# Kernel tuning notes

Measured on AMD Instinct MI355X. Metric: run time of the kernel, lower is better.

The kernel has to match this reference:

```python
import jax, jax.numpy as jnp
import numpy as np

N_NODES = 100000
N_EDGES = 1600000
IN_DIM = 16
HID = 128
N_LAYERS = 3
LN_EPS = 1e-5


def setup_inputs() -> dict:
    key = jax.random.key(0)
    ks = jax.random.split(key, 8)
    x = jax.random.normal(ks[0], (N_NODES, IN_DIM), dtype=jnp.float32)
    edge_index = jax.random.randint(ks[1], (2, N_EDGES), 0, N_NODES, dtype=jnp.int64)
    # input projection params
    W_in = jax.random.normal(ks[2], (IN_DIM, HID), dtype=jnp.float32) * (1.0 / np.sqrt(IN_DIM))
    b_in = jnp.zeros((HID,), dtype=jnp.float32)
    # stacked GCNConv weights [L, H, H] and biases [L, H]
    W_conv = jax.random.normal(ks[3], (N_LAYERS, HID, HID), dtype=jnp.float32) * (1.0 / np.sqrt(HID))
    b_conv = jnp.zeros((N_LAYERS, HID), dtype=jnp.float32)
    # LayerNorm params [L, H]
    ln_gamma = jnp.ones((N_LAYERS, HID), dtype=jnp.float32)
    ln_beta = jnp.zeros((N_LAYERS, HID), dtype=jnp.float32)
    return {"x": x, "edge_index": edge_index, "W_in": W_in, "b_in": b_in,
            "W_conv": W_conv, "b_conv": b_conv, "ln_gamma": ln_gamma, "ln_beta": ln_beta}


def _layer_norm(h, gamma, beta):
    mu = jnp.mean(h, axis=-1, keepdims=True)
    var = jnp.mean(jnp.square(h - mu), axis=-1, keepdims=True)
    return (h - mu) * jax.lax.rsqrt(var + LN_EPS) * gamma + beta


def reference(x, edge_index, W_in, b_in, W_conv, b_conv, ln_gamma, ln_beta):
    N = x.shape[0]
    loops = jnp.arange(N, dtype=edge_index.dtype)
    src = jnp.concatenate([edge_index[0], loops])  # add self-loops (GCNConv default)
    dst = jnp.concatenate([edge_index[1], loops])
    # symmetric normalization D^-1/2 (A+I) D^-1/2
    deg = jax.ops.segment_sum(jnp.ones(src.shape[0], dtype=x.dtype), dst, num_segments=N)
    dis = jax.lax.rsqrt(jnp.maximum(deg, 1.0))  # deg >= 1 with self-loops
    coef = (dis[src] * dis[dst])[:, None]  # [E+N, 1]
    h = x @ W_in + b_in  # input projection -> [N, HID]
    for l in range(N_LAYERS):
        h_prev = h
        m = h @ W_conv[l]  # transform then propagate (same math as GCNConv)
        agg = jax.ops.segment_sum(m[src] * coef, dst, num_segments=N) + b_conv[l]
        h = jax.nn.relu(_layer_norm(agg, ln_gamma[l], ln_beta[l]))
        if l > 0:  # residual only for i > 0, dims always match
            h = h + h_prev
    return h
```

## Files before the change

### kernel.cpp

```cpp
#include <hip/hip_runtime.h>
#include <hip/hip_bf16.h>
#include <hip/hip_fp16.h>

#define HID 128
#define BCHUNK 4096

typedef __attribute__((ext_vector_type(8))) short short8;
typedef __attribute__((ext_vector_type(4))) float f32x4;

__device__ __forceinline__ float ldf(const void* p, size_t i, int bf16f) {
    if (bf16f) {
        unsigned short u = ((const unsigned short*)p)[i];
        union { unsigned int x; float f; } v; v.x = ((unsigned int)u) << 16;
        return v.f;
    }
    return ((const float*)p)[i];
}
__device__ __forceinline__ int ld_idx(const void* p, size_t i, int i64f) {
    return i64f ? (int)((const long long*)p)[i] : ((const int*)p)[i];
}
__device__ __forceinline__ unsigned short f2bfu(float f) {
    __hip_bfloat16 h = __float2bfloat16(f);
    return *reinterpret_cast<unsigned short*>(&h);
}
__device__ __forceinline__ float bfbits(unsigned int lo16) {
    union { unsigned int x; float f; } v; v.x = lo16 << 16;
    return v.f;
}

__global__ void k_detect(const void* __restrict__ gamma, const void* __restrict__ ei,
                         int* flags) {
    if (threadIdx.x == 0 && blockIdx.x == 0) {
        unsigned int g0 = ((const unsigned int*)gamma)[0];
        flags[0] = (g0 != 0x3F800000u) ? 1 : 0;
        const unsigned int* e32 = (const unsigned int*)ei;
        int i64 = 1;
        for (int k = 0; k < 128; k++)
            if (e32[2 * k + 1] != 0u) { i64 = 0; break; }
        flags[1] = i64;
    }
}

__global__ void k_zero(int* p, int n) {
    int i = blockIdx.x * blockDim.x + threadIdx.x;
    if (i < n) p[i] = 0;
}

__global__ __launch_bounds__(256) void k_bucket(const void* __restrict__ ei,
                                                int E, int N, int nbk, int cap,
                                                int* bkcur, unsigned* __restrict__ bdata,
                                                const int* __restrict__ flags) {
    __shared__ int hist[512], base[512];
    int i64 = flags[1];
    int t = threadIdx.x;
    for (int i = t; i < nbk; i += 256) hist[i] = 0;
    __syncthreads();
    int e0 = blockIdx.x * BCHUNK;
    int ss[16], dd[16];
#pragma unroll
    for (int k = 0; k < 16; k++) {
        int e = e0 + k * 256 + t;
        dd[k] = -1;
        if (e < E) {
            int d = ld_idx(ei, (size_t)E + e, i64);
            int s = ld_idx(ei, e, i64);
            if ((unsigned)d < (unsigned)N && (unsigned)s < (unsigned)N) {
                dd[k] = d; ss[k] = s;
                atomicAdd(&hist[d >> 9], 1);
            }
        }
    }
    __syncthreads();
    for (int i = t; i < nbk; i += 256) {
        int c = hist[i];
        base[i] = c ? atomicAdd(&bkcur[i], c) : 0;
        hist[i] = 0;
    }
    __syncthreads();
#pragma unroll
    for (int k = 0; k < 16; k++) {
        if (dd[k] >= 0) {
            int b = dd[k] >> 9;
            int pos = base[b] + atomicAdd(&hist[b], 1);
            if (pos < cap)
                bdata[(size_t)b * cap + pos] =
                    (unsigned)ss[k] | ((unsigned)(dd[k] & 511) << 17);
        }
    }
}

__global__ void k_bkscan(const int* __restrict__ bkcur, int* bkpre, int nbk,
                         int* row_ptr, int N, int cap) {
    if (threadIdx.x == 0 && blockIdx.x == 0) {
        int run = 0;
        for (int b = 0; b < nbk; b++) {
            bkpre[b] = run;
            run += min(bkcur[b], cap);
        }
        row_ptr[N] = run;
    }
}

__global__ __launch_bounds__(256) void k_bhist(const int* __restrict__ bkcur,
                                               const int* __restrict__ bkpre,
                                               const unsigned* __restrict__ bdata,
                                               int cap, int* __restrict__ row_ptr,
                                               float* __restrict__ dis, int N) {
    __shared__ int hist[512];
    __shared__ int lsum;
    int b = blockIdx.x, t = threadIdx.x;
    for (int i = t; i < 512; i += 256) hist[i] = 0;
    __syncthreads();
    int cb = min(bkcur[b], cap);
    for (int k = t; k < cb; k += 256)
        atomicAdd(&hist[bdata[(size_t)b * cap + k] >> 17], 1);
    __syncthreads();
    int v0 = hist[t], v1 = hist[256 + t];
    int s0 = v0, s1 = v1;
    for (int off = 1; off < 256; off <<= 1) {
        int x0 = (t >= off) ? hist[t - off] : 0;
        int x1 = (t >= off) ? hist[256 + t - off] : 0;
        __syncthreads();
        s0 += x0; s1 += x1;
        hist[t] = s0; hist[256 + t] = s1;
        __syncthreads();
    }
    if (t == 255) lsum = s0;
    __syncthreads();
    int nbase = b << 9;
    int base = bkpre[b];
    if (nbase + t < N) {
        row_ptr[nbase + t] = base + s0 - v0;
        dis[nbase + t] = rsqrtf((float)(v0 + 1));
    }
    if (nbase + 256 + t < N) {
        row_ptr[nbase + 256 + t] = base + lsum + s1 - v1;
        dis[nbase + 256 + t] = rsqrtf((float)(v1 + 1));
    }
}

__global__ __launch_bounds__(256) void k_bfill(const int* __restrict__ bkcur,
                                               const unsigned* __restrict__ bdata,
                                               int cap, const int* __restrict__ row_ptr,
                                               int* __restrict__ csr_src, int N) {
    __shared__ int cur[512];
    int b = blockIdx.x, t = threadIdx.x;
    for (int i = t; i < 512; i += 256) cur[i] = 0;
    __syncthreads();
    int cb = min(bkcur[b], cap);
    int nbase = b << 9;
    for (int k = t; k < cb; k += 256) {
        unsigned u = bdata[(size_t)b * cap + k];
        int dl = u >> 17;
        int j = row_ptr[nbase + dl] + atomicAdd(&cur[dl], 1);
        csr_src[j] = (int)(u & 0x1FFFFu);
    }
}

__global__ void k_wtrans(const void* __restrict__ W, unsigned short* __restrict__ Wt,
                         const int* __restrict__ flags) {
    int bf = flags[0];
    int l = blockIdx.x >> 7, n = blockIdx.x & 127, k = threadIdx.x;
    float w = ldf(W, (size_t)l * 16384 + (size_t)k * 128 + n, bf);
    Wt[(size_t)l * 16384 + (size_t)n * 128 + k] = f2bfu(w);
}

__global__ void k_proj(const void* __restrict__ x, const void* __restrict__ Win,
                       const void* __restrict__ bin,
                       unsigned short* __restrict__ hb, int N,
                       const int* __restrict__ flags) {
    int bf = flags[0];
    int node = blockIdx.x;
    int t = threadIdx.x;
    __shared__ float xs[16];
    if (t < 16) xs[t] = ldf(x, (size_t)node * 16 + t, bf);
    __syncthreads();
    float acc = ldf(bin, t, bf);
#pragma unroll
    for (int k = 0; k < 16; k++)
        acc += xs[k] * ldf(Win, (size_t)k * HID + t, bf);
    hb[(size_t)node * HID + t] = f2bfu(acc);
}

__global__ __launch_bounds__(256) void k_gemm(const unsigned short* __restrict__ hb,
                                              const unsigned short* __restrict__ Wt,
                                              unsigned short* __restrict__ m, int N,
                                              int ntiles) {
    int t = threadIdx.x;
    int wave = t >> 6, lane = t & 63;
    int quad = lane >> 4, n15 = lane & 15;
    short8 bfr[4][8];
#pragma unroll
    for (int kc = 0; kc < 4; kc++)
#pragma unroll
        for (int nt = 0; nt < 8; nt++)
            bfr[kc][nt] = *(const short8*)(Wt + (size_t)(nt * 16 + n15) * HID +
                                           kc * 32 + quad * 8);
    int wid = blockIdx.x * 4 + wave;
    int nwaves = gridDim.x * 4;
    for (int tile = wid; tile < ntiles; tile += nwaves) {
        int row0 = tile * 16;
        int arow = min(row0 + n15, N - 1);
        const short8* ap = (const short8*)(hb + (size_t)arow * HID + quad * 8);
        short8 a0 = ap[0], a1 = ap[4], a2 = ap[8], a3 = ap[12];
        f32x4 acc[8] = {};
#pragma unroll
        for (int nt = 0; nt < 8; nt++) {
            acc[nt] = __builtin_amdgcn_mfma_f32_16x16x32_bf16(a0, bfr[0][nt], acc[nt], 0, 0, 0);
            acc[nt] = __builtin_amdgcn_mfma_f32_16x16x32_bf16(a1, bfr[1][nt], acc[nt], 0, 0, 0);
            acc[nt] = __builtin_amdgcn_mfma_f32_16x16x32_bf16(a2, bfr[2][nt], acc[nt], 0, 0, 0);
            acc[nt] = __builtin_amdgcn_mfma_f32_16x16x32_bf16(a3, bfr[3][nt], acc[nt], 0, 0, 0);
        }
#pragma unroll
        for (int nt = 0; nt < 8; nt++)
#pragma unroll
            for (int r = 0; r < 4; r++) {
                int row = row0 + quad * 4 + r;
                if (row < N)
                    m[(size_t)row * HID + nt * 16 + n15] = f2bfu(acc[nt][r]);
            }
    }
}

__global__ __launch_bounds__(256) void k_layer(
        const int* __restrict__ row_ptr, const int* __restrict__ csr_src,
        const unsigned int* __restrict__ m2, const float* __restrict__ dis,
        const void* __restrict__ bc, size_t boff,
        const void* __restrict__ lg, const void* __restrict__ lb, size_t goff,
        unsigned int* __restrict__ hb, void* __restrict__ out, int N,
        int res, int last, const int* __restrict__ flags) {
    int t = threadIdx.x, wave = t >> 6, lane = t & 63;
    int node = blockIdx.x * 4 + wave;
    if (node >= N) return;
    int bf = flags[0];
    float dn = dis[node], dd = dn * dn;
    unsigned int ms = m2[(size_t)node * 64 + lane];
    float v0 = ldf(bc, boff + 2 * lane, bf)     + bfbits(ms & 0xffffu) * dd;
    float v1 = ldf(bc, boff + 2 * lane + 1, bf) + bfbits(ms >> 16) * dd;
    int beg = row_ptr[node], end = row_ptr[node + 1];
    float p0 = 0.f, p1 = 0.f, q0 = 0.f, q1 = 0.f, r0 = 0.f, r1 = 0.f;
    int j = beg;
    for (; j + 3 < end; j += 4) {
        int s0 = csr_src[j], s1 = csr_src[j + 1];
        int s2 = csr_src[j + 2], s3 = csr_src[j + 3];
        float c0 = dis[s0] * dn, c1 = dis[s1] * dn;
        float c2 = dis[s2] * dn, c3 = dis[s3] * dn;
        unsigned int u0 = m2[(size_t)s0 * 64 + lane];
        unsigned int u1 = m2[(size_t)s1 * 64 + lane];
        unsigned int u2 = m2[(size_t)s2 * 64 + lane];
        unsigned int u3 = m2[(size_t)s3 * 64 + lane];
        v0 += bfbits(u0 & 0xffffu) * c0; v1 += bfbits(u0 >> 16) * c0;
        p0 += bfbits(u1 & 0xffffu) * c1; p1 += bfbits(u1 >> 16) * c1;
        q0 += bfbits(u2 & 0xffffu) * c2; q1 += bfbits(u2 >> 16) * c2;
        r0 += bfbits(u3 & 0xffffu) * c3; r1 += bfbits(u3 >> 16) * c3;
    }
    for (; j < end; j++) {
        int s0 = csr_src[j];
        float c0 = dis[s0] * dn;
        unsigned int u0 = m2[(size_t)s0 * 64 + lane];
        v0 += bfbits(u0 & 0xffffu) * c0; v1 += bfbits(u0 >> 16) * c0;
    }
    v0 += p0 + q0 + r0;
    v1 += p1 + q1 + r1;
    float s1 = v0 + v1, s2 = v0 * v0 + v1 * v1;
#pragma unroll
    for (int o = 32; o; o >>= 1) {
        s1 += __shfl_down(s1, o);
        s2 += __shfl_down(s2, o);
    }
    float sum = __shfl(s1, 0), sq = __shfl(s2, 0);
    float mu = sum * (1.0f / HID);
    float var = sq * (1.0f / HID) - mu * mu;
    float r = rsqrtf(var + 1e-5f);
    float g0 = ldf(lg, goff + 2 * lane, bf), g1 = ldf(lg, goff + 2 * lane + 1, bf);
    float b0 = ldf(lb, goff + 2 * lane, bf), b1 = ldf(lb, goff + 2 * lane + 1, bf);
    float o0 = fmaxf((v0 - mu) * r * g0 + b0, 0.f);
    float o1 = fmaxf((v1 - mu) * r * g1 + b1, 0.f);
    size_t widx = (size_t)node * 64 + lane;
    if (res) {
        unsigned int hp = hb[widx];
        o0 += bfbits(hp & 0xffffu);
        o1 += bfbits(hp >> 16);
    }
    unsigned int packed = (unsigned int)f2bfu(o0) | ((unsigned int)f2bfu(o1) << 16);
    hb[widx] = packed;
    if (last) {
        if (bf) ((unsigned int*)out)[widx] = packed;
        else {
            size_t base = (size_t)node * HID + 2 * lane;
            *(float2*)&((float*)out)[base] = make_float2(o0, o1);
        }
    }
}

extern "C" void kernel_launch(void* const* d_in, const int* in_sizes, int n_in,
                              void* d_out, int out_size, void* d_ws, size_t ws_size,
                              hipStream_t stream) {
    const void* x   = d_in[0];
    const void* ei  = d_in[1];
    const void* Win = d_in[2];
    const void* bin = d_in[3];
    const void* Wc  = d_in[4];
    const void* bc  = d_in[5];
    const void* lg  = d_in[6];
    const void* lb  = d_in[7];

    int N = in_sizes[0] / 16;
    int E = in_sizes[1] / 2;
    int nbk = (N + 511) >> 9;
    int cap = ((E / nbk) * 2 + 255) & ~255;

    char* ws = (char*)d_ws;
    size_t off = 0;
    auto alloc = [&](size_t bytes) {
        void* p = ws + off;
        off += (bytes + 255) / 256 * 256;
        return p;
    };
    int*            flags    = (int*)alloc(256);
    float*          dis      = (float*)alloc((size_t)N * 4);
    int*            row_ptr  = (int*)alloc(((size_t)N + 1) * 4);
    int*            bkcur    = (int*)alloc((size_t)nbk * 4);
    int*            bkpre    = (int*)alloc((size_t)nbk * 4);
    unsigned*       bdata    = (unsigned*)alloc((size_t)nbk * cap * 4);
    int*            csr_src  = (int*)alloc((size_t)E * 4);
    unsigned short* hb       = (unsigned short*)alloc((size_t)N * HID * 2);
    unsigned short* m        = (unsigned short*)alloc((size_t)N * HID * 2);
    unsigned short* Wt       = (unsigned short*)alloc((size_t)3 * HID * HID * 2);
    (void)ws_size;

    k_detect<<<1, 64, 0, stream>>>(lg, ei, flags);
    k_zero<<<(nbk + 255) / 256, 256, 0, stream>>>(bkcur, nbk);
    k_bucket<<<(E + BCHUNK - 1) / BCHUNK, 256, 0, stream>>>(ei, E, N, nbk, cap,
                                                            bkcur, bdata, flags);
    k_bkscan<<<1, 64, 0, stream>>>(bkcur, bkpre, nbk, row_ptr, N, cap);
    k_bhist<<<nbk, 256, 0, stream>>>(bkcur, bkpre, bdata, cap, row_ptr, dis, N);
    k_bfill<<<nbk, 256, 0, stream>>>(bkcur, bdata, cap, row_ptr, csr_src, N);
    k_wtrans<<<3 * HID, HID, 0, stream>>>(Wc, Wt, flags);
    k_proj<<<N, HID, 0, stream>>>(x, Win, bin, hb, N, flags);

    int ntiles = (N + 15) / 16;
    int lblocks = (N + 3) / 4;
    for (int l = 0; l < 3; l++) {
        k_gemm<<<512, 256, 0, stream>>>(hb, Wt + (size_t)l * HID * HID, m, N, ntiles);
        k_layer<<<lblocks, 256, 0, stream>>>(row_ptr, csr_src,
                                             (const unsigned int*)m, dis, bc,
                                             (size_t)l * HID, lg, lb, (size_t)l * HID,
                                             (unsigned int*)hb, d_out, N,
                                             l > 0, l == 2, flags);
    }
}
```

Before: 503.5 us.

## Precompute per-edge coefficients into packed CSR and merge small setup kernels

```diff
diff --git a/kernel.cpp b/kernel.cpp
--- a/kernel.cpp
+++ b/kernel.cpp
@@ -28,9 +28,11 @@
     return v.f;
 }
 
-__global__ void k_detect(const void* __restrict__ gamma, const void* __restrict__ ei,
-                         int* flags) {
-    if (threadIdx.x == 0 && blockIdx.x == 0) {
+__global__ void k_init(const void* __restrict__ gamma, const void* __restrict__ ei,
+                       int* flags, int* bkcur, int nbk) {
+    int t = threadIdx.x;
+    for (int i = t; i < nbk; i += 256) bkcur[i] = 0;
+    if (t == 0) {
         unsigned int g0 = ((const unsigned int*)gamma)[0];
         flags[0] = (g0 != 0x3F800000u) ? 1 : 0;
         const unsigned int* e32 = (const unsigned int*)ei;
@@ -39,11 +41,6 @@
             if (e32[2 * k + 1] != 0u) { i64 = 0; break; }
         flags[1] = i64;
     }
-}
-
-__global__ void k_zero(int* p, int n) {
-    int i = blockIdx.x * blockDim.x + threadIdx.x;
-    if (i < n) p[i] = 0;
 }
 
 __global__ __launch_bounds__(256) void k_bucket(const void* __restrict__ ei,
@@ -142,7 +139,8 @@
 __global__ __launch_bounds__(256) void k_bfill(const int* __restrict__ bkcur,
                                                const unsigned* __restrict__ bdata,
                                                int cap, const int* __restrict__ row_ptr,
-                                               int* __restrict__ csr_src, int N) {
+                                               const float* __restrict__ dis,
+                                               uint2* __restrict__ csr, int N) {
     __shared__ int cur[512];
     int b = blockIdx.x, t = threadIdx.x;
     for (int i = t; i < 512; i += 256) cur[i] = 0;
@@ -151,27 +149,30 @@
     int nbase = b << 9;
     for (int k = t; k < cb; k += 256) {
         unsigned u = bdata[(size_t)b * cap + k];
-        int dl = u >> 17;
-        int j = row_ptr[nbase + dl] + atomicAdd(&cur[dl], 1);
-        csr_src[j] = (int)(u & 0x1FFFFu);
-    }
-}
-
-__global__ void k_wtrans(const void* __restrict__ W, unsigned short* __restrict__ Wt,
-                         const int* __restrict__ flags) {
-    int bf = flags[0];
-    int l = blockIdx.x >> 7, n = blockIdx.x & 127, k = threadIdx.x;
-    float w = ldf(W, (size_t)l * 16384 + (size_t)k * 128 + n, bf);
-    Wt[(size_t)l * 16384 + (size_t)n * 128 + k] = f2bfu(w);
+        int dl = (int)(u >> 17);
+        int s = (int)(u & 0x1FFFFu);
+        int d = nbase + dl;
+        int j = row_ptr[d] + atomicAdd(&cur[dl], 1);
+        float c = dis[s] * dis[d];
+        csr[j] = make_uint2((unsigned)s, __float_as_uint(c));
+    }
 }
 
 __global__ void k_proj(const void* __restrict__ x, const void* __restrict__ Win,
                        const void* __restrict__ bin,
                        unsigned short* __restrict__ hb, int N,
+                       const void* __restrict__ Wc, unsigned short* __restrict__ Wt,
                        const int* __restrict__ flags) {
     int bf = flags[0];
+    int t = threadIdx.x;
+    if (blockIdx.x >= N) {
+        int i = blockIdx.x - N;
+        int l = i >> 7, n = i & 127;
+        float w = ldf(Wc, (size_t)l * 16384 + (size_t)t * 128 + n, bf);
+        Wt[(size_t)l * 16384 + (size_t)n * 128 + t] = f2bfu(w);
+        return;
+    }
     int node = blockIdx.x;
-    int t = threadIdx.x;
     __shared__ float xs[16];
     if (t < 16) xs[t] = ldf(x, (size_t)node * 16 + t, bf);
     __syncthreads();
@@ -223,7 +224,7 @@
 }
 
 __global__ __launch_bounds__(256) void k_layer(
-        const int* __restrict__ row_ptr, const int* __restrict__ csr_src,
+        const int* __restrict__ row_ptr, const uint2* __restrict__ csr,
         const unsigned int* __restrict__ m2, const float* __restrict__ dis,
         const void* __restrict__ bc, size_t boff,
         const void* __restrict__ lg, const void* __restrict__ lb, size_t goff,
@@ -241,23 +242,22 @@
     float p0 = 0.f, p1 = 0.f, q0 = 0.f, q1 = 0.f, r0 = 0.f, r1 = 0.f;
     int j = beg;
     for (; j + 3 < end; j += 4) {
-        int s0 = csr_src[j], s1 = csr_src[j + 1];
-        int s2 = csr_src[j + 2], s3 = csr_src[j + 3];
-        float c0 = dis[s0] * dn, c1 = dis[s1] * dn;
-        float c2 = dis[s2] * dn, c3 = dis[s3] * dn;
-        unsigned int u0 = m2[(size_t)s0 * 64 + lane];
-        unsigned int u1 = m2[(size_t)s1 * 64 + lane];
-        unsigned int u2 = m2[(size_t)s2 * 64 + lane];
-        unsigned int u3 = m2[(size_t)s3 * 64 + lane];
+        uint2 e0 = csr[j], e1 = csr[j + 1], e2 = csr[j + 2], e3 = csr[j + 3];
+        unsigned int u0 = m2[(size_t)e0.x * 64 + lane];
+        unsigned int u1 = m2[(size_t)e1.x * 64 + lane];
+        unsigned int u2 = m2[(size_t)e2.x * 64 + lane];
+        unsigned int u3 = m2[(size_t)e3.x * 64 + lane];
+        float c0 = __uint_as_float(e0.y), c1 = __uint_as_float(e1.y);
+        float c2 = __uint_as_float(e2.y), c3 = __uint_as_float(e3.y);
         v0 += bfbits(u0 & 0xffffu) * c0; v1 += bfbits(u0 >> 16) * c0;
         p0 += bfbits(u1 & 0xffffu) * c1; p1 += bfbits(u1 >> 16) * c1;
         q0 += bfbits(u2 & 0xffffu) * c2; q1 += bfbits(u2 >> 16) * c2;
         r0 += bfbits(u3 & 0xffffu) * c3; r1 += bfbits(u3 >> 16) * c3;
     }
     for (; j < end; j++) {
-        int s0 = csr_src[j];
-        float c0 = dis[s0] * dn;
-        unsigned int u0 = m2[(size_t)s0 * 64 + lane];
+        uint2 e0 = csr[j];
+        unsigned int u0 = m2[(size_t)e0.x * 64 + lane];
+        float c0 = __uint_as_float(e0.y);
         v0 += bfbits(u0 & 0xffffu) * c0; v1 += bfbits(u0 >> 16) * c0;
     }
     v0 += p0 + q0 + r0;
@@ -323,27 +323,25 @@
     int*            bkcur    = (int*)alloc((size_t)nbk * 4);
     int*            bkpre    = (int*)alloc((size_t)nbk * 4);
     unsigned*       bdata    = (unsigned*)alloc((size_t)nbk * cap * 4);
-    int*            csr_src  = (int*)alloc((size_t)E * 4);
+    uint2*          csr      = (uint2*)alloc((size_t)E * 8);
     unsigned short* hb       = (unsigned short*)alloc((size_t)N * HID * 2);
     unsigned short* m        = (unsigned short*)alloc((size_t)N * HID * 2);
     unsigned short* Wt       = (unsigned short*)alloc((size_t)3 * HID * HID * 2);
     (void)ws_size;
 
-    k_detect<<<1, 64, 0, stream>>>(lg, ei, flags);
-    k_zero<<<(nbk + 255) / 256, 256, 0, stream>>>(bkcur, nbk);
+    k_init<<<1, 256, 0, stream>>>(lg, ei, flags, bkcur, nbk);
     k_bucket<<<(E + BCHUNK - 1) / BCHUNK, 256, 0, stream>>>(ei, E, N, nbk, cap,
                                                             bkcur, bdata, flags);
     k_bkscan<<<1, 64, 0, stream>>>(bkcur, bkpre, nbk, row_ptr, N, cap);
     k_bhist<<<nbk, 256, 0, stream>>>(bkcur, bkpre, bdata, cap, row_ptr, dis, N);
-    k_bfill<<<nbk, 256, 0, stream>>>(bkcur, bdata, cap, row_ptr, csr_src, N);
-    k_wtrans<<<3 * HID, HID, 0, stream>>>(Wc, Wt, flags);
-    k_proj<<<N, HID, 0, stream>>>(x, Win, bin, hb, N, flags);
+    k_bfill<<<nbk, 256, 0, stream>>>(bkcur, bdata, cap, row_ptr, dis, csr, N);
+    k_proj<<<N + 3 * HID, HID, 0, stream>>>(x, Win, bin, hb, N, Wc, Wt, flags);
 
     int ntiles = (N + 15) / 16;
     int lblocks = (N + 3) / 4;
     for (int l = 0; l < 3; l++) {
         k_gemm<<<512, 256, 0, stream>>>(hb, Wt + (size_t)l * HID * HID, m, N, ntiles);
-        k_layer<<<lblocks, 256, 0, stream>>>(row_ptr, csr_src,
+        k_layer<<<lblocks, 256, 0, stream>>>(row_ptr, csr,
                                              (const unsigned int*)m, dis, bc,
                                              (size_t)l * HID, lg, lb, (size_t)l * HID,
                                              (unsigned int*)hb, d_out, N,
```

Measured after the change: 516.3 us. 2.6% more time.

## Fuse CSR build kernels and merge weight transpose into projection launch

Applied to the files above, without the earlier changes.

```diff
diff --git a/kernel.cpp b/kernel.cpp
--- a/kernel.cpp
+++ b/kernel.cpp
@@ -28,9 +28,11 @@
     return v.f;
 }
 
-__global__ void k_detect(const void* __restrict__ gamma, const void* __restrict__ ei,
-                         int* flags) {
-    if (threadIdx.x == 0 && blockIdx.x == 0) {
+__global__ void k_init(const void* __restrict__ gamma, const void* __restrict__ ei,
+                       int* flags, int* bkcur, int nbk) {
+    int t = threadIdx.x;
+    for (int i = t; i < nbk; i += 256) bkcur[i] = 0;
+    if (t == 0) {
         unsigned int g0 = ((const unsigned int*)gamma)[0];
         flags[0] = (g0 != 0x3F800000u) ? 1 : 0;
         const unsigned int* e32 = (const unsigned int*)ei;
@@ -39,11 +41,6 @@
             if (e32[2 * k + 1] != 0u) { i64 = 0; break; }
         flags[1] = i64;
     }
-}
-
-__global__ void k_zero(int* p, int n) {
-    int i = blockIdx.x * blockDim.x + threadIdx.x;
-    if (i < n) p[i] = 0;
 }
 
 __global__ __launch_bounds__(256) void k_bucket(const void* __restrict__ ei,
@@ -89,26 +86,28 @@
     }
 }
 
-__global__ void k_bkscan(const int* __restrict__ bkcur, int* bkpre, int nbk,
-                         int* row_ptr, int N, int cap) {
-    if (threadIdx.x == 0 && blockIdx.x == 0) {
-        int run = 0;
-        for (int b = 0; b < nbk; b++) {
-            bkpre[b] = run;
-            run += min(bkcur[b], cap);
-        }
-        row_ptr[N] = run;
-    }
-}
-
-__global__ __launch_bounds__(256) void k_bhist(const int* __restrict__ bkcur,
-                                               const int* __restrict__ bkpre,
-                                               const unsigned* __restrict__ bdata,
-                                               int cap, int* __restrict__ row_ptr,
-                                               float* __restrict__ dis, int N) {
+__global__ __launch_bounds__(256) void k_bfused(const int* __restrict__ bkcur,
+                                                const unsigned* __restrict__ bdata,
+                                                int cap, int* __restrict__ row_ptr,
+                                                float* __restrict__ dis,
+                                                int* __restrict__ csr_src,
+                                                int N, int nbk) {
     __shared__ int hist[512];
-    __shared__ int lsum;
+    __shared__ int sb[256];
+    __shared__ int lsum, bkbase;
     int b = blockIdx.x, t = threadIdx.x;
+    int bv = (t < nbk) ? min(bkcur[t], cap) : 0;
+    sb[t] = bv;
+    __syncthreads();
+    int acc = bv;
+    for (int off = 1; off < 256; off <<= 1) {
+        int x = (t >= off) ? sb[t - off] : 0;
+        __syncthreads();
+        acc += x; sb[t] = acc;
+        __syncthreads();
+    }
+    if (t == b) bkbase = acc - bv;
+    if (b == nbk - 1 && t == nbk - 1) row_ptr[N] = acc;
     for (int i = t; i < 512; i += 256) hist[i] = 0;
     __syncthreads();
     int cb = min(bkcur[b], cap);
@@ -128,50 +127,41 @@
     if (t == 255) lsum = s0;
     __syncthreads();
     int nbase = b << 9;
-    int base = bkpre[b];
+    int e0 = bkbase + s0 - v0;
+    int e1 = bkbase + lsum + s1 - v1;
     if (nbase + t < N) {
-        row_ptr[nbase + t] = base + s0 - v0;
+        row_ptr[nbase + t] = e0;
         dis[nbase + t] = rsqrtf((float)(v0 + 1));
     }
     if (nbase + 256 + t < N) {
-        row_ptr[nbase + 256 + t] = base + lsum + s1 - v1;
+        row_ptr[nbase + 256 + t] = e1;
         dis[nbase + 256 + t] = rsqrtf((float)(v1 + 1));
     }
-}
-
-__global__ __launch_bounds__(256) void k_bfill(const int* __restrict__ bkcur,
-                                               const unsigned* __restrict__ bdata,
-                                               int cap, const int* __restrict__ row_ptr,
-                                               int* __restrict__ csr_src, int N) {
-    __shared__ int cur[512];
-    int b = blockIdx.x, t = threadIdx.x;
-    for (int i = t; i < 512; i += 256) cur[i] = 0;
-    __syncthreads();
-    int cb = min(bkcur[b], cap);
-    int nbase = b << 9;
+    __syncthreads();
+    hist[t] = e0; hist[256 + t] = e1;
+    __syncthreads();
     for (int k = t; k < cb; k += 256) {
         unsigned u = bdata[(size_t)b * cap + k];
-        int dl = u >> 17;
-        int j = row_ptr[nbase + dl] + atomicAdd(&cur[dl], 1);
+        int j = atomicAdd(&hist[u >> 17], 1);
         csr_src[j] = (int)(u & 0x1FFFFu);
     }
-}
-
-__global__ void k_wtrans(const void* __restrict__ W, unsigned short* __restrict__ Wt,
-                         const int* __restrict__ flags) {
-    int bf = flags[0];
-    int l = blockIdx.x >> 7, n = blockIdx.x & 127, k = threadIdx.x;
-    float w = ldf(W, (size_t)l * 16384 + (size_t)k * 128 + n, bf);
-    Wt[(size_t)l * 16384 + (size_t)n * 128 + k] = f2bfu(w);
 }
 
 __global__ void k_proj(const void* __restrict__ x, const void* __restrict__ Win,
                        const void* __restrict__ bin,
                        unsigned short* __restrict__ hb, int N,
+                       const void* __restrict__ Wc, unsigned short* __restrict__ Wt,
                        const int* __restrict__ flags) {
     int bf = flags[0];
+    int t = threadIdx.x;
+    if (blockIdx.x >= N) {
+        int i = blockIdx.x - N;
+        int l = i >> 7, n = i & 127;
+        float w = ldf(Wc, (size_t)l * 16384 + (size_t)t * 128 + n, bf);
+        Wt[(size_t)l * 16384 + (size_t)n * 128 + t] = f2bfu(w);
+        return;
+    }
     int node = blockIdx.x;
-    int t = threadIdx.x;
     __shared__ float xs[16];
     if (t < 16) xs[t] = ldf(x, (size_t)node * 16 + t, bf);
     __syncthreads();
@@ -321,7 +311,6 @@
     float*          dis      = (float*)alloc((size_t)N * 4);
     int*            row_ptr  = (int*)alloc(((size_t)N + 1) * 4);
     int*            bkcur    = (int*)alloc((size_t)nbk * 4);
-    int*            bkpre    = (int*)alloc((size_t)nbk * 4);
     unsigned*       bdata    = (unsigned*)alloc((size_t)nbk * cap * 4);
     int*            csr_src  = (int*)alloc((size_t)E * 4);
     unsigned short* hb       = (unsigned short*)alloc((size_t)N * HID * 2);
@@ -329,15 +318,12 @@
     unsigned short* Wt       = (unsigned short*)alloc((size_t)3 * HID * HID * 2);
     (void)ws_size;
 
-    k_detect<<<1, 64, 0, stream>>>(lg, ei, flags);
-    k_zero<<<(nbk + 255) / 256, 256, 0, stream>>>(bkcur, nbk);
+    k_init<<<1, 256, 0, stream>>>(lg, ei, flags, bkcur, nbk);
     k_bucket<<<(E + BCHUNK - 1) / BCHUNK, 256, 0, stream>>>(ei, E, N, nbk, cap,
                                                             bkcur, bdata, flags);
-    k_bkscan<<<1, 64, 0, stream>>>(bkcur, bkpre, nbk, row_ptr, N, cap);
-    k_bhist<<<nbk, 256, 0, stream>>>(bkcur, bkpre, bdata, cap, row_ptr, dis, N);
-    k_bfill<<<nbk, 256, 0, stream>>>(bkcur, bdata, cap, row_ptr, csr_src, N);
-    k_wtrans<<<3 * HID, HID, 0, stream>>>(Wc, Wt, flags);
-    k_proj<<<N, HID, 0, stream>>>(x, Win, bin, hb, N, flags);
+    k_bfused<<<nbk, 256, 0, stream>>>(bkcur, bdata, cap, row_ptr, dis, csr_src,
+                                      N, nbk);
+    k_proj<<<N + 3 * HID, HID, 0, stream>>>(x, Win, bin, hb, N, Wc, Wt, flags);
 
     int ntiles = (N + 15) / 16;
     int lblocks = (N + 3) / 4;
```

Result: faster. 493.4 us (-2.0%).
